# Kernel tuning notes

Hardware: AMD Instinct MI355X
Metric: run time of the kernel (lower is better)

The kernel has to match this reference:

```python
import jax, jax.numpy as jnp
import numpy as np

C = 256; GC = 32; G = C // GC; K = 3; S = 1; NEW = 2; PAD = (K - 1) // 2
IN1 = C * K * 2 + C * K * K // 32          # 1608
OUT1 = G * NEW * NEW * K * K // 4          # 72
OUT2 = G * NEW * NEW * K * K               # 288
B = 8; H = 56; W = 56


def setup_inputs():
    key = jax.random.key(0)
    k0, k1, k2 = jax.random.split(key, 3)
    inputs = jax.random.normal(k0, (B, C, H, W), jnp.float32)
    W1 = jax.random.normal(k1, (OUT1, IN1), jnp.float32) * np.float32(1.0 / np.sqrt(IN1))
    b1 = jnp.zeros((OUT1,), jnp.float32)
    W2 = jax.random.normal(k2, (OUT2, OUT1), jnp.float32) * np.float32(1.0 / np.sqrt(OUT1))
    b2 = jnp.zeros((OUT2,), jnp.float32)
    return {"inputs": inputs, "W1": W1, "b1": b1, "W2": W2, "b2": b2}


def _unfold(x, h, w):
    # torch.nn.Unfold(K, 1, PAD, S): patches of shape (B, C, K, K, h, w)
    xp = jnp.pad(x, ((0, 0), (0, 0), (PAD, PAD), (PAD, PAD)))
    cols = [xp[:, :, di:di + (h - 1) * S + 1:S, dj:dj + (w - 1) * S + 1:S]
            for di in range(K) for dj in range(K)]  # fixed K*K=9 slices
    return jnp.stack(cols, axis=2).reshape(x.shape[0], x.shape[1], K, K, h, w)


def reference(inputs, W1, b1, W2, b2):
    b, c, Hh, Ww = inputs.shape
    h = (Hh + 2 * PAD - K) // S + 1
    w = (Ww + 2 * PAD - K) // S + 1
    # (B, G, GC, K, K, h, w)
    x = _unfold(inputs, h, w).reshape(b, G, GC, K, K, h, w)
    # three max-pooled descriptors over different axes
    x1 = x.reshape(b, G, -1, GC // 32, K, K, h, w).max(axis=2).reshape(b, -1, h, w)  # (B, C*K*K//32, h, w)
    x2 = x.max(axis=3).reshape(b, -1, h, w)  # (B, C*K, h, w)
    x3 = x.max(axis=4).reshape(b, -1, h, w)  # (B, C*K, h, w)
    feat = jnp.concatenate([x1, x2, x3], axis=1)  # (B, IN1, h, w)
    # two biased 1x1 convs (ConvModule with no norm/act)
    y = jnp.einsum('bchw,oc->bohw', feat, W1) + b1[None, :, None, None]
    y = jnp.einsum('bchw,oc->bohw', y, W2) + b2[None, :, None, None]
    # softmax over the K*K kernel-window dim
    wgt = jax.nn.softmax(y.reshape(b, G, K * K, NEW * NEW, h, w), axis=2)
    # softmax-weighted local aggregation: sum over kernel window
    agg = jnp.einsum('bgckhw,bgknhw->bgcnhw', x.reshape(b, G, GC, K * K, h, w), wgt)
    # fold with non-overlapping (NEW, NEW) blocks == block upsampling reshape
    return agg.reshape(b, C, NEW, NEW, h, w).transpose(0, 1, 4, 2, 5, 3).reshape(b, C, h * NEW, w * NEW)
```

## Files before the change

kernel.cpp:

```cpp
#include <hip/hip_runtime.h>

#define CC   256
#define HH   56
#define WWID 56
#define KIN1 1608
#define KP1  1632
#define NO1  72
#define NO2  288
#define PPB  14
#define H2   112
#define W2D  112

typedef unsigned short u16;
typedef unsigned int   u32;
typedef __attribute__((ext_vector_type(8))) short v8s;
typedef __attribute__((ext_vector_type(4))) float v4f;

#define W1BF_ELEMS (80 * KP1)
#define W2BF_OFF_B 262144

#define LDS_TOTAL 32768
#define OFF_A 0
#define OFF_B 21504
#define OFF_C 29696

#define Y2S 300

#define SWZ(row) (((row) & 7) << 3)

__device__ __forceinline__ u16 f2b(float x) {
  u32 u = __float_as_uint(x);
  u = (u + 0x7FFFu + ((u >> 16) & 1u)) >> 16;
  return (u16)u;
}

#define DPPMAX(m, ctrl)                                                          \
  do {                                                                           \
    int _y = __builtin_amdgcn_update_dpp(0, __float_as_int(m), (ctrl), 0xF, 0xF, false); \
    (m) = fmaxf((m), __int_as_float(_y));                                        \
  } while (0)

__global__ void kConvW(const float* __restrict__ W1, const float* __restrict__ W2,
                       u16* __restrict__ w1bf, u16* __restrict__ w2bf) {
  int idx = blockIdx.x * 256 + threadIdx.x;
  if (idx < W1BF_ELEMS) {
    int m = idx / KP1, k = idx - m * KP1;
    float v = 0.f;
    if (m < NO1) {
      int orig = -1;
      if (k < 768)                 orig = 72 + (k & 255) * 3 + (k >> 8);
      else if (k < 1536)           orig = 840 + (k & 255) * 3 + ((k - 768) >> 8);
      else if ((k - 1536) < NO1)   orig = k - 1536;
      if (orig >= 0) v = W1[m * KIN1 + orig];
    }
    w1bf[idx] = f2b(v);
  } else {
    int i2 = idx - W1BF_ELEMS;
    if (i2 < NO2 * 96) {
      int m = i2 / 96, k = i2 - m * 96;
      w2bf[i2] = (k < NO1) ? f2b(W2[m * NO1 + k]) : (u16)0;
    }
  }
}

__global__ __launch_bounds__(256, 4)
void kFused(const float* __restrict__ in, const u16* __restrict__ w1bf,
            const float* __restrict__ b1, const u16* __restrict__ w2bf,
            const float* __restrict__ b2, float* __restrict__ out) {
  __shared__ __align__(16) char lds[LDS_TOTAL];
  u16*   rowmaxT = (u16*)(lds + OFF_A);
  u16*   colmaxT = (u16*)(lds + OFF_B);
  u16*   x1T     = (u16*)(lds + OFF_C);
  float* partA   = (float*)(lds + OFF_A);
  float* y2L     = (float*)(lds + OFF_A);
  float* tile    = (float*)(lds + OFF_A);

  const int t  = threadIdx.x;
  const int L  = blockIdx.x + 4 * (blockIdx.y + 56 * blockIdx.z);
  const int jq = L >> 3;
  const int jt = jq & 3, i = jq >> 2, b = L & 7;
  const int c  = t;
  const int g  = c >> 5;
  const int gc = c & 31;
  const int w  = t >> 6, lane = t & 63;
  const int ml = lane & 15, quad = lane >> 4;

  {
    u32* xu = (u32*)x1T;
    if (t < 132) {
#pragma unroll
      for (int rp2 = 0; rp2 < 2; ++rp2) {
        int idx = 2 * t + rp2;
        if (idx < 192) {
          int row = idx / 12;
          xu[(row * 48 + 36 + (idx - row * 12)) ^ ((row & 7) << 2)] = 0u;
        } else {
          int e = idx - 192, row = 14 + e / 36;
          xu[(row * 48 + (e % 36)) ^ ((row & 7) << 2)] = 0u;
        }
      }
    }
  }

  const float* rowbase0 = in + ((size_t)b * CC + c) * (HH * WWID);
  u32 win_p[3][8];
  float colmax[16];
#pragma unroll
  for (int k = 0; k < 16; ++k) colmax[k] = -3.0e38f;

#pragma unroll
  for (int r = 0; r < 3; ++r) {
    const int row = i - 1 + r;
    float sc[16];
    if (row < 0 || row >= HH) {
#pragma unroll
      for (int k = 0; k < 16; ++k) sc[k] = 0.f;
    } else {
      const float* rp = rowbase0 + row * WWID;
      float l[20];
      if (jt == 0) {
        const float4 a0 = *(const float4*)(rp), a1 = *(const float4*)(rp + 4),
                     a2 = *(const float4*)(rp + 8), a3 = *(const float4*)(rp + 12);
        l[0]=a0.x;l[1]=a0.y;l[2]=a0.z;l[3]=a0.w; l[4]=a1.x;l[5]=a1.y;l[6]=a1.z;l[7]=a1.w;
        l[8]=a2.x;l[9]=a2.y;l[10]=a2.z;l[11]=a2.w; l[12]=a3.x;l[13]=a3.y;l[14]=a3.z;l[15]=a3.w;
        sc[0] = 0.f;
#pragma unroll
        for (int k = 1; k < 16; ++k) sc[k] = l[k - 1];
      } else if (jt == 3) {
        const float* q = rp + 40;
        const float4 a0 = *(const float4*)(q), a1 = *(const float4*)(q + 4),
                     a2 = *(const float4*)(q + 8), a3 = *(const float4*)(q + 12);
        l[0]=a0.x;l[1]=a0.y;l[2]=a0.z;l[3]=a0.w; l[4]=a1.x;l[5]=a1.y;l[6]=a1.z;l[7]=a1.w;
        l[8]=a2.x;l[9]=a2.y;l[10]=a2.z;l[11]=a2.w; l[12]=a3.x;l[13]=a3.y;l[14]=a3.z;l[15]=a3.w;
#pragma unroll
        for (int k = 0; k < 15; ++k) sc[k] = l[k + 1];
        sc[15] = 0.f;
      } else {
        const float* q = rp + ((jt == 1) ? 12 : 24);
        const float4 a0 = *(const float4*)(q), a1 = *(const float4*)(q + 4),
                     a2 = *(const float4*)(q + 8), a3 = *(const float4*)(q + 12),
                     a4 = *(const float4*)(q + 16);
        l[0]=a0.x;l[1]=a0.y;l[2]=a0.z;l[3]=a0.w; l[4]=a1.x;l[5]=a1.y;l[6]=a1.z;l[7]=a1.w;
        l[8]=a2.x;l[9]=a2.y;l[10]=a2.z;l[11]=a2.w; l[12]=a3.x;l[13]=a3.y;l[14]=a3.z;l[15]=a3.w;
        l[16]=a4.x;l[17]=a4.y;l[18]=a4.z;l[19]=a4.w;
        if (jt == 1) {
#pragma unroll
          for (int k = 0; k < 16; ++k) sc[k] = l[k + 1];
        } else {
#pragma unroll
          for (int k = 0; k < 16; ++k) sc[k] = l[k + 3];
        }
      }
    }
#pragma unroll
    for (int k = 0; k < 16; ++k) colmax[k] = fmaxf(colmax[k], sc[k]);
#pragma unroll
    for (int n = 0; n < 14; ++n)
      rowmaxT[(n * 768 + r * 256 + c) ^ SWZ(n)] =
          f2b(fmaxf(fmaxf(sc[n], sc[n + 1]), sc[n + 2]));
#pragma unroll
    for (int col = 0; col < 16; ++col) {
      float m = sc[col];
      DPPMAX(m, 0xB1);
      DPPMAX(m, 0x4E);
      DPPMAX(m, 0x141);
      DPPMAX(m, 0x140);
      { int y = __builtin_amdgcn_ds_swizzle(__float_as_int(m), 0x401F);
        m = fmaxf(m, __int_as_float(y)); }
      if (gc == col) {
        u16 mv = f2b(m);
#pragma unroll
        for (int kj = 0; kj < 3; ++kj) {
          const int n = col - kj;
          if (n >= 0 && n < 14)
            x1T[(n * 96 + g * 9 + r * 3 + kj) ^ SWZ(n)] = mv;
        }
      }
    }
#pragma unroll
    for (int k = 0; k < 8; ++k)
      win_p[r][k] = (u32)f2b(sc[2 * k]) | ((u32)f2b(sc[2 * k + 1]) << 16);
  }
#pragma unroll
  for (int col = 0; col < 16; ++col)
    colmaxT[(col * 256 + c) ^ SWZ(col)] = f2b(colmax[col]);
  __syncthreads();

  v4f acc[5];
#pragma unroll
  for (int mt = 0; mt < 5; ++mt) acc[mt] = (v4f){0.f, 0.f, 0.f, 0.f};
  const int ks0 = w * 13, ks1 = (w == 3) ? 51 : ks0 + 13;

  auto loadB = [&](int ks) -> v8s {
    if (ks < 24) {
      int kj = ks >> 3, c0 = (ks & 7) * 32, rowi = ml + kj;
      return *(v8s*)&colmaxT[(rowi * 256 + c0 + quad * 8) ^ SWZ(rowi)];
    } else if (ks < 48) {
      return *(v8s*)&rowmaxT[(ml * 768 + (ks - 24) * 32 + quad * 8) ^ SWZ(ml)];
    } else {
      return *(v8s*)&x1T[(ml * 96 + (ks - 48) * 32 + quad * 8) ^ SWZ(ml)];
    }
  };

  {
    v8s bf_c = loadB(ks0);
    v8s af_c[5];
    {
      const int k0 = ks0 * 32 + quad * 8;
#pragma unroll
      for (int mt = 0; mt < 5; ++mt)
        af_c[mt] = *(const v8s*)&w1bf[(mt * 16 + ml) * KP1 + k0];
    }
    for (int ks = ks0; ks < ks1; ++ks) {
      v8s bf_n, af_n[5];
      if (ks + 1 < ks1) {
        bf_n = loadB(ks + 1);
        const int k0n = (ks + 1) * 32 + quad * 8;
#pragma unroll
        for (int mt = 0; mt < 5; ++mt)
          af_n[mt] = *(const v8s*)&w1bf[(mt * 16 + ml) * KP1 + k0n];
      }
#pragma unroll
      for (int mt = 0; mt < 5; ++mt)
        acc[mt] = __builtin_amdgcn_mfma_f32_16x16x32_bf16(af_c[mt], bf_c, acc[mt], 0, 0, 0);
      if (ks + 1 < ks1) {
        bf_c = bf_n;
#pragma unroll
        for (int mt = 0; mt < 5; ++mt) af_c[mt] = af_n[mt];
      }
    }
  }
  __syncthreads();

#pragma unroll
  for (int mt = 0; mt < 5; ++mt)
    *(v4f*)&partA[((w * 5 + mt) * 16 + ml) * 16 + quad * 4] = acc[mt];
  __syncthreads();

  u16* y1b = x1T;
#pragma unroll
  for (int it = 0; it < 4; ++it) {
    int e = t + it * 256;
    if (e < NO1 * PPB) {
      int m = e / PPB, n = e - m * PPB;
      float s = b1[m];
#pragma unroll
      for (int ww = 0; ww < 4; ++ww)
        s += partA[((ww * 5 + (m >> 4)) * 16 + n) * 16 + (m & 15)];
      y1b[(n * 96 + m) ^ SWZ(n)] = f2b(s);
    }
  }
  __syncthreads();

  {
    v8s bfr[3];
#pragma unroll
    for (int ks = 0; ks < 3; ++ks)
      bfr[ks] = *(v8s*)&y1b[(ml * 96 + ks * 32 + quad * 8) ^ SWZ(ml)];
    const int mt0 = (w < 2) ? 5 * w : 10 + 4 * (w - 2);
    const int mtn = (w < 2) ? 5 : 4;
    const u16* w2base = w2bf + ml * 96 + quad * 8;
    v8s afA[3], afB[3];
#pragma unroll
    for (int ks = 0; ks < 3; ++ks)
      afA[ks] = *(const v8s*)(w2base + (mt0 * 16) * 96 + ks * 32);
#pragma unroll
    for (int mi = 0; mi < 5; ++mi) {
      if (mi < mtn) {
        const int mt = mt0 + mi;
        v4f a2 = (v4f){0.f, 0.f, 0.f, 0.f};
        if ((mi & 1) == 0) {
          if (mi + 1 < mtn) {
#pragma unroll
            for (int ks = 0; ks < 3; ++ks)
              afB[ks] = *(const v8s*)(w2base + ((mt + 1) * 16) * 96 + ks * 32);
          }
#pragma unroll
          for (int ks = 0; ks < 3; ++ks)
            a2 = __builtin_amdgcn_mfma_f32_16x16x32_bf16(afA[ks], bfr[ks], a2, 0, 0, 0);
        } else {
          if (mi + 1 < mtn) {
#pragma unroll
            for (int ks = 0; ks < 3; ++ks)
              afA[ks] = *(const v8s*)(w2base + ((mt + 1) * 16) * 96 + ks * 32);
          }
#pragma unroll
          for (int ks = 0; ks < 3; ++ks)
            a2 = __builtin_amdgcn_mfma_f32_16x16x32_bf16(afB[ks], bfr[ks], a2, 0, 0, 0);
        }
        const int o0 = mt * 16 + quad * 4;
        const float4 bv = *(const float4*)(b2 + o0);
        a2[0] += bv.x; a2[1] += bv.y; a2[2] += bv.z; a2[3] += bv.w;
        *(v4f*)&y2L[ml * Y2S + o0] = a2;
      }
    }
  }
  __syncthreads();

#pragma unroll
  for (int it = 0; it < 2; ++it) {
    int s2 = t + it * 256;
    if (s2 < 448) {
      int gg = s2 / 56, rem = s2 - gg * 56, nn = rem / PPB, n = rem - nn * PPB;
      float* bp = &y2L[n * Y2S + gg * 36 + nn];
      float v9[9], m = -1e30f;
#pragma unroll
      for (int k = 0; k < 9; ++k) { v9[k] = bp[k * 4]; m = fmaxf(m, v9[k]); }
      float sum = 0.f;
#pragma unroll
      for (int k = 0; k < 9; ++k) { v9[k] = __expf(v9[k] - m); sum += v9[k]; }
      float inv = 1.f / sum;
#pragma unroll
      for (int k = 0; k < 9; ++k) bp[k * 4] = v9[k] * inv;
    }
  }
  __syncthreads();

  float a0s[14], a1s[14], a2s[14], a3s[14];
#pragma unroll
  for (int n = 0; n < 14; ++n) {
    const v4f* wp = (const v4f*)&y2L[n * Y2S + g * 36];
    float a0 = 0.f, a1 = 0.f, a2v = 0.f, a3 = 0.f;
#pragma unroll
    for (int r = 0; r < 3; ++r) {
      float x0, x1, x2v;
      if ((n & 1) == 0) {
        u32 ua = win_p[r][n >> 1], ub = win_p[r][(n >> 1) + 1];
        x0  = __uint_as_float(ua << 16);
        x1  = __uint_as_float(ua & 0xffff0000u);
        x2v = __uint_as_float(ub << 16);
      } else {
        u32 ua = win_p[r][n >> 1], ub = win_p[r][(n >> 1) + 1];
        x0  = __uint_as_float(ua & 0xffff0000u);
        x1  = __uint_as_float(ub << 16);
        x2v = __uint_as_float(ub & 0xffff0000u);
      }
#pragma unroll
      for (int kj = 0; kj < 3; ++kj) {
        v4f wv = wp[r * 3 + kj];
        float x = (kj == 0) ? x0 : (kj == 1) ? x1 : x2v;
        a0  = fmaf(x, wv[0], a0);
        a1  = fmaf(x, wv[1], a1);
        a2v = fmaf(x, wv[2], a2v);
        a3  = fmaf(x, wv[3], a3);
      }
    }
    a0s[n] = a0; a1s[n] = a1; a2s[n] = a2v; a3s[n] = a3;
  }
  __syncthreads();

  const int cl = c & 63;
  for (int ch = 0; ch < 4; ++ch) {
    if ((c >> 6) == ch) {
#pragma unroll
      for (int n = 0; n < 14; ++n) {
        float2 lo2; lo2.x = a0s[n]; lo2.y = a1s[n];
        float2 hi2; hi2.x = a2s[n]; hi2.y = a3s[n];
        *(float2*)&tile[cl * 60 + 2 * n] = lo2;
        *(float2*)&tile[cl * 60 + 28 + 2 * n] = hi2;
      }
    }
    __syncthreads();
#pragma unroll
    for (int it = 0; it < 4; ++it) {
      int f = t + it * 256;
      if (f < 896) {
        int rr = f / 7, xi = f - rr * 7;
        int cg = ch * 64 + (rr >> 1), di = rr & 1;
        v4f val = *(v4f*)&tile[(rr >> 1) * 60 + di * 28 + xi * 4];
        *(v4f*)&out[((size_t)(b * CC + cg) * H2 + (size_t)(2 * i + di)) * W2D
                    + 28 * jt + xi * 4] = val;
      }
    }
    __syncthreads();
  }
}

extern "C" void kernel_launch(void* const* d_in, const int* in_sizes, int n_in,
                              void* d_out, int out_size, void* d_ws, size_t ws_size,
                              hipStream_t stream) {
  const float* in = (const float*)d_in[0];
  const float* W1 = (const float*)d_in[1];
  const float* b1 = (const float*)d_in[2];
  const float* W2 = (const float*)d_in[3];
  const float* b2 = (const float*)d_in[4];
  float* out = (float*)d_out;

  u16* w1bf = (u16*)d_ws;
  u16* w2bf = (u16*)((char*)d_ws + W2BF_OFF_B);

  const int B = in_sizes[0] / (CC * HH * WWID);

  kConvW<<<dim3((W1BF_ELEMS + NO2 * 96 + 255) / 256), 256, 0, stream>>>(W1, W2, w1bf, w2bf);
  dim3 grid(WWID / PPB, HH, B);
  kFused<<<grid, 256, 0, stream>>>(in, w1bf, b1, w2bf, b2, out);
}
```

Before: 201.2 us.

## Hoist input row loads, pack weight conversion pairs, raise MFMA wave priority

The three input rows are now loaded up front into registers, so all global loads are in flight before any max-pooling work starts. Previously each row was loaded and then processed in turn. The weight-conversion kernel now produces two bf16 values per thread and writes them as one 32-bit store, which halves its grid. s_setprio is raised around the MFMA blocks in both GEMMs to favour matrix-issuing waves. These are separate ideas that cost extra registers (60 floats held live) and may lower occupancy.

```diff
diff --git a/kernel.cpp b/kernel.cpp
--- a/kernel.cpp
+++ b/kernel.cpp
@@ -42,23 +42,35 @@
 
 __global__ void kConvW(const float* __restrict__ W1, const float* __restrict__ W2,
                        u16* __restrict__ w1bf, u16* __restrict__ w2bf) {
-  int idx = blockIdx.x * 256 + threadIdx.x;
-  if (idx < W1BF_ELEMS) {
-    int m = idx / KP1, k = idx - m * KP1;
-    float v = 0.f;
+  int p = blockIdx.x * 256 + threadIdx.x;
+  int e0 = 2 * p;
+  float v0 = 0.f, v1 = 0.f;
+  if (e0 < W1BF_ELEMS) {
+    int m = e0 / KP1, k = e0 - m * KP1;
     if (m < NO1) {
-      int orig = -1;
-      if (k < 768)                 orig = 72 + (k & 255) * 3 + (k >> 8);
-      else if (k < 1536)           orig = 840 + (k & 255) * 3 + ((k - 768) >> 8);
-      else if ((k - 1536) < NO1)   orig = k - 1536;
-      if (orig >= 0) v = W1[m * KIN1 + orig];
-    }
-    w1bf[idx] = f2b(v);
+      const float* Wm = W1 + m * KIN1;
+      if (k < 768) {
+        int o = 72 + (k & 255) * 3 + (k >> 8);
+        v0 = Wm[o]; v1 = Wm[o + 3];
+      } else if (k < 1536) {
+        int o = 840 + (k & 255) * 3 + ((k - 768) >> 8);
+        v0 = Wm[o]; v1 = Wm[o + 3];
+      } else {
+        int t1 = k - 1536;
+        if (t1 < NO1)     v0 = Wm[t1];
+        if (t1 + 1 < NO1) v1 = Wm[t1 + 1];
+      }
+    }
+    ((u32*)w1bf)[p] = (u32)f2b(v0) | ((u32)f2b(v1) << 16);
   } else {
-    int i2 = idx - W1BF_ELEMS;
+    int i2 = e0 - W1BF_ELEMS;
     if (i2 < NO2 * 96) {
       int m = i2 / 96, k = i2 - m * 96;
-      w2bf[i2] = (k < NO1) ? f2b(W2[m * NO1 + k]) : (u16)0;
+      if (k < NO1) {
+        v0 = W2[m * NO1 + k];
+        if (k + 1 < NO1) v1 = W2[m * NO1 + k + 1];
+      }
+      ((u32*)w2bf)[i2 >> 1] = (u32)f2b(v0) | ((u32)f2b(v1) << 16);
     }
   }
 }
@@ -103,6 +115,39 @@
   }
 
   const float* rowbase0 = in + ((size_t)b * CC + c) * (HH * WWID);
+  float l3[3][20];
+#pragma unroll
+  for (int r = 0; r < 3; ++r) {
+    const int row = i - 1 + r;
+    if (row < 0 || row >= HH) {
+#pragma unroll
+      for (int k = 0; k < 20; ++k) l3[r][k] = 0.f;
+    } else {
+      const float* rp = rowbase0 + row * WWID;
+      if (jt == 0) {
+        *(float4*)&l3[r][0]  = *(const float4*)(rp);
+        *(float4*)&l3[r][4]  = *(const float4*)(rp + 4);
+        *(float4*)&l3[r][8]  = *(const float4*)(rp + 8);
+        *(float4*)&l3[r][12] = *(const float4*)(rp + 12);
+        l3[r][16] = l3[r][17] = l3[r][18] = l3[r][19] = 0.f;
+      } else if (jt == 3) {
+        const float* q = rp + 40;
+        *(float4*)&l3[r][0]  = *(const float4*)(q);
+        *(float4*)&l3[r][4]  = *(const float4*)(q + 4);
+        *(float4*)&l3[r][8]  = *(const float4*)(q + 8);
+        *(float4*)&l3[r][12] = *(const float4*)(q + 12);
+        l3[r][16] = l3[r][17] = l3[r][18] = l3[r][19] = 0.f;
+      } else {
+        const float* q = rp + ((jt == 1) ? 12 : 24);
+        *(float4*)&l3[r][0]  = *(const float4*)(q);
+        *(float4*)&l3[r][4]  = *(const float4*)(q + 4);
+        *(float4*)&l3[r][8]  = *(const float4*)(q + 8);
+        *(float4*)&l3[r][12] = *(const float4*)(q + 12);
+        *(float4*)&l3[r][16] = *(const float4*)(q + 16);
+      }
+    }
+  }
+
   u32 win_p[3][8];
   float colmax[16];
 #pragma unroll
@@ -110,47 +155,21 @@
 
 #pragma unroll
   for (int r = 0; r < 3; ++r) {
-    const int row = i - 1 + r;
     float sc[16];
-    if (row < 0 || row >= HH) {
-#pragma unroll
-      for (int k = 0; k < 16; ++k) sc[k] = 0.f;
+    if (jt == 0) {
+      sc[0] = 0.f;
+#pragma unroll
+      for (int k = 1; k < 16; ++k) sc[k] = l3[r][k - 1];
+    } else if (jt == 3) {
+#pragma unroll
+      for (int k = 0; k < 15; ++k) sc[k] = l3[r][k + 1];
+      sc[15] = 0.f;
+    } else if (jt == 1) {
+#pragma unroll
+      for (int k = 0; k < 16; ++k) sc[k] = l3[r][k + 1];
     } else {
-      const float* rp = rowbase0 + row * WWID;
-      float l[20];
-      if (jt == 0) {
-        const float4 a0 = *(const float4*)(rp), a1 = *(const float4*)(rp + 4),
-                     a2 = *(const float4*)(rp + 8), a3 = *(const float4*)(rp + 12);
-        l[0]=a0.x;l[1]=a0.y;l[2]=a0.z;l[3]=a0.w; l[4]=a1.x;l[5]=a1.y;l[6]=a1.z;l[7]=a1.w;
-        l[8]=a2.x;l[9]=a2.y;l[10]=a2.z;l[11]=a2.w; l[12]=a3.x;l[13]=a3.y;l[14]=a3.z;l[15]=a3.w;
-        sc[0] = 0.f;
-#pragma unroll
-        for (int k = 1; k < 16; ++k) sc[k] = l[k - 1];
-      } else if (jt == 3) {
-        const float* q = rp + 40;
-        const float4 a0 = *(const float4*)(q), a1 = *(const float4*)(q + 4),
-                     a2 = *(const float4*)(q + 8), a3 = *(const float4*)(q + 12);
-        l[0]=a0.x;l[1]=a0.y;l[2]=a0.z;l[3]=a0.w; l[4]=a1.x;l[5]=a1.y;l[6]=a1.z;l[7]=a1.w;
-        l[8]=a2.x;l[9]=a2.y;l[10]=a2.z;l[11]=a2.w; l[12]=a3.x;l[13]=a3.y;l[14]=a3.z;l[15]=a3.w;
-#pragma unroll
-        for (int k = 0; k < 15; ++k) sc[k] = l[k + 1];
-        sc[15] = 0.f;
-      } else {
-        const float* q = rp + ((jt == 1) ? 12 : 24);
-        const float4 a0 = *(const float4*)(q), a1 = *(const float4*)(q + 4),
-                     a2 = *(const float4*)(q + 8), a3 = *(const float4*)(q + 12),
-                     a4 = *(const float4*)(q + 16);
-        l[0]=a0.x;l[1]=a0.y;l[2]=a0.z;l[3]=a0.w; l[4]=a1.x;l[5]=a1.y;l[6]=a1.z;l[7]=a1.w;
-        l[8]=a2.x;l[9]=a2.y;l[10]=a2.z;l[11]=a2.w; l[12]=a3.x;l[13]=a3.y;l[14]=a3.z;l[15]=a3.w;
-        l[16]=a4.x;l[17]=a4.y;l[18]=a4.z;l[19]=a4.w;
-        if (jt == 1) {
-#pragma unroll
-          for (int k = 0; k < 16; ++k) sc[k] = l[k + 1];
-        } else {
-#pragma unroll
-          for (int k = 0; k < 16; ++k) sc[k] = l[k + 3];
-        }
-      }
+#pragma unroll
+      for (int k = 0; k < 16; ++k) sc[k] = l3[r][k + 3];
     }
 #pragma unroll
     for (int k = 0; k < 16; ++k) colmax[k] = fmaxf(colmax[k], sc[k]);
@@ -220,9 +239,11 @@
         for (int mt = 0; mt < 5; ++mt)
           af_n[mt] = *(const v8s*)&w1bf[(mt * 16 + ml) * KP1 + k0n];
       }
+      __builtin_amdgcn_s_setprio(1);
 #pragma unroll
       for (int mt = 0; mt < 5; ++mt)
         acc[mt] = __builtin_amdgcn_mfma_f32_16x16x32_bf16(af_c[mt], bf_c, acc[mt], 0, 0, 0);
+      __builtin_amdgcn_s_setprio(0);
       if (ks + 1 < ks1) {
         bf_c = bf_n;
 #pragma unroll
@@ -275,18 +296,22 @@
             for (int ks = 0; ks < 3; ++ks)
               afB[ks] = *(const v8s*)(w2base + ((mt + 1) * 16) * 96 + ks * 32);
           }
+          __builtin_amdgcn_s_setprio(1);
 #pragma unroll
           for (int ks = 0; ks < 3; ++ks)
             a2 = __builtin_amdgcn_mfma_f32_16x16x32_bf16(afA[ks], bfr[ks], a2, 0, 0, 0);
+          __builtin_amdgcn_s_setprio(0);
         } else {
           if (mi + 1 < mtn) {
 #pragma unroll
             for (int ks = 0; ks < 3; ++ks)
               afA[ks] = *(const v8s*)(w2base + ((mt + 1) * 16) * 96 + ks * 32);
           }
+          __builtin_amdgcn_s_setprio(1);
 #pragma unroll
           for (int ks = 0; ks < 3; ++ks)
             a2 = __builtin_amdgcn_mfma_f32_16x16x32_bf16(afB[ks], bfr[ks], a2, 0, 0, 0);
+          __builtin_amdgcn_s_setprio(0);
         }
         const int o0 = mt * 16 + quad * 4;
         const float4 bv = *(const float4*)(b2 + o0);
@@ -391,7 +416,7 @@
 
   const int B = in_sizes[0] / (CC * HH * WWID);
 
-  kConvW<<<dim3((W1BF_ELEMS + NO2 * 96 + 255) / 256), 256, 0, stream>>>(W1, W2, w1bf, w2bf);
+  kConvW<<<dim3(((W1BF_ELEMS + NO2 * 96) / 2 + 255) / 256), 256, 0, stream>>>(W1, W2, w1bf, w2bf);
   dim3 grid(WWID / PPB, HH, B);
   kFused<<<grid, 256, 0, stream>>>(in, w1bf, b1, w2bf, b2, out);
 }
```

Measured after the change: 194.4 us. -3.4%, faster.
